# Optimization experiments

Hardware: AMD Instinct MI355X
Metric: run time of the kernel (lower is better)

The kernel has to match this reference:

```python
import jax, jax.numpy as jnp
from jax import lax
import numpy as np

CH = [1, 64, 64, 128, 128, 256, 256, 256, 512, 512, 512, 512, 512, 512]
POOL_AFTER = {2, 4, 7, 10, 13}  # VGG16: pool after layers 2,4,7,10,13
FLAT = 512 * 16 * 16  # 131072 after 5 pools of 512x512
MLP_DIMS = [(FLAT, 1024), (1024, 512), (512, 256), (256, 2)]


def _conv(x, w, b):
    # x: [B,C,H,W], w: [O,I,3,3] (OIHW), SAME padding, stride 1
    y = lax.conv_general_dilated(x, w, (1, 1), 'SAME',
                                 dimension_numbers=('NCHW', 'OIHW', 'NCHW'))
    return y + b[None, :, None, None]


def _pool(x):
    return lax.reduce_window(x, -jnp.inf, lax.max, (1, 1, 2, 2), (1, 1, 2, 2), 'VALID')


def setup_inputs() -> dict:
    key = jax.random.key(0)
    ks = jax.random.split(key, 40)
    inp = {}
    xr = jax.random.normal(ks[0], (2, 1, 512, 512), jnp.float32)
    keep = (jax.random.uniform(ks[1], (2, 1, 512, 512)) < 0.05).astype(jnp.float32)
    inp['x'] = xr * keep
    for i in range(13):
        cin, cout = CH[i], CH[i + 1]
        inp[f'w{i+1}'] = jax.random.normal(ks[2 + i], (cout, cin, 3, 3), jnp.float32) / np.sqrt(cin * 9.0)
        inp[f'b{i+1}'] = jnp.zeros((cout,), jnp.float32)
    for j, (a, b) in enumerate(MLP_DIMS):
        inp[f'fw{j+1}'] = jax.random.normal(ks[20 + j], (b, a), jnp.float32) / np.sqrt(float(a))
        inp[f'fb{j+1}'] = jnp.zeros((b,), jnp.float32)
    return inp


def reference(x, w1, b1, w2, b2, w3, b3, w4, b4, w5, b5, w6, b6, w7, b7,
              w8, b8, w9, b9, w10, b10, w11, b11, w12, b12, w13, b13,
              fw1, fb1, fw2, fb2, fw3, fb3, fw4, fb4):
    ws = [w1, w2, w3, w4, w5, w6, w7, w8, w9, w10, w11, w12, w13]
    bs = [b1, b2, b3, b4, b5, b6, b7, b8, b9, b10, b11, b12, b13]
    # active-site mask from nonzero input (spconv SparseConvTensor.from_dense)
    m = jnp.any(x != 0, axis=1, keepdims=True).astype(x.dtype)  # [B,1,H,W]
    h = x
    for i in range(13):
        # SubMConv2d: conv output (incl. bias) exists only at active sites -> mask
        h = jax.nn.relu(_conv(h, ws[i], bs[i]) * m)
        if (i + 1) in POOL_AFTER:
            # sparse maxpool == dense maxpool here (features >=0, inactive == 0)
            h = _pool(h)
            m = _pool(m)
    h = h.reshape(h.shape[0], -1)  # [B, 131072]
    h = jax.nn.relu(h @ fw1.T + fb1)
    h = jax.nn.relu(h @ fw2.T + fb2)
    h = jax.nn.relu(h @ fw3.T + fb3)
    return h @ fw4.T + fb4  # [B, 2]
```

## Files before the change

### kernel.cpp

```cpp
#include <hip/hip_runtime.h>
#include <hip/hip_bf16.h>
#include <cstddef>
#include <cstdint>

#define NB 2

#define NMAX512 32768
#define NMAX256 28672
#define NMAX128 20480
#define NMAX64  8192
#define NMAX32  2048

typedef __attribute__((ext_vector_type(8))) short bf8v;
typedef __attribute__((ext_vector_type(4))) float f32x4;
typedef __attribute__((ext_vector_type(16))) float f32x16;

static __device__ __forceinline__ unsigned short f2bf(float x) {
  __hip_bfloat16 h = __float2bfloat16(x);
  return *reinterpret_cast<unsigned short*>(&h);
}
static __device__ __forceinline__ float bf2f(unsigned short u) {
  __hip_bfloat16 h;
  *reinterpret_cast<unsigned short*>(&h) = u;
  return __bfloat162float(h);
}

__global__ __launch_bounds__(256) void build_l0_k(const float* __restrict__ x,
    int* __restrict__ list, int* __restrict__ im, float* __restrict__ f0,
    int* __restrict__ nact, int total, int nmax) {
  int i = blockIdx.x * 256 + threadIdx.x;
  bool act = false;
  float v = 0.f;
  if (i < total) { v = x[i]; act = (v != 0.f); }
  unsigned long long mb = __ballot(act);
  int lane = threadIdx.x & 63;
  int prefix = __popcll(mb & ((1ull << lane) - 1));
  int base = 0;
  if (lane == 0) base = atomicAdd(nact, __popcll(mb));
  base = __shfl(base, 0);
  if (i < total) {
    int idx = act ? (base + prefix) : -1;
    if (idx >= nmax) idx = -1;
    im[i] = idx;
    if (idx >= 0) {
      int b = i >> 18;
      int rem = i & 262143;
      list[idx] = (b << 20) | ((rem >> 9) << 10) | (rem & 511);
      f0[idx] = v;
    }
  }
}

__global__ __launch_bounds__(256) void build_pl_k(const int* __restrict__ imF,
    int* __restrict__ list, int* __restrict__ im, int* __restrict__ nact,
    int Hc, int nmax) {
  int total = NB * Hc * Hc;
  int i = blockIdx.x * 256 + threadIdx.x;
  bool act = false;
  int b = 0, y = 0, x = 0;
  int Hf = Hc * 2;
  if (i < total) {
    x = i % Hc; y = (i / Hc) % Hc; b = i / (Hc * Hc);
    const int* p = imF + ((size_t)b * Hf + 2 * y) * Hf + 2 * x;
    act = (p[0] >= 0) || (p[1] >= 0) || (p[Hf] >= 0) || (p[Hf + 1] >= 0);
  }
  unsigned long long mb = __ballot(act);
  int lane = threadIdx.x & 63;
  int prefix = __popcll(mb & ((1ull << lane) - 1));
  int base = 0;
  if (lane == 0) base = atomicAdd(nact, __popcll(mb));
  base = __shfl(base, 0);
  if (i < total) {
    int idx = act ? (base + prefix) : -1;
    if (idx >= nmax) idx = -1;
    im[i] = idx;
    if (idx >= 0) list[idx] = (b << 20) | (y << 10) | x;
  }
}

__global__ __launch_bounds__(256) void build_nbr_k(const int* __restrict__ list,
    const int* __restrict__ im, const int* __restrict__ nactp,
    int* __restrict__ nbr, int H, int nmax) {
  int i = blockIdx.x * 256 + threadIdx.x;
  if (i >= nactp[0]) return;
  int code = list[i];
  int b = code >> 20, y = (code >> 10) & 1023, x = code & 1023;
#pragma unroll
  for (int k = 0; k < 9; ++k) {
    int yy = y + k / 3 - 1, xx = x + k % 3 - 1;
    int v = -1;
    if (yy >= 0 && yy < H && xx >= 0 && xx < H)
      v = im[((size_t)b * H + yy) * H + xx];
    nbr[k * nmax + i] = v;
  }
}

__global__ __launch_bounds__(256) void transpose_k(const float* __restrict__ in,
                                                   float* __restrict__ out,
                                                   int R, int C) {
  __shared__ float tile[32][33];
  int bx = blockIdx.x * 32;
  int by = blockIdx.y * 32;
  int tx = threadIdx.x % 32, ty0 = threadIdx.x / 32;
  for (int ty = ty0; ty < 32; ty += 8) {
    int r = by + ty, c = bx + tx;
    tile[ty][tx] = (r < R && c < C) ? in[(size_t)r * C + c] : 0.f;
  }
  __syncthreads();
  for (int ty = ty0; ty < 32; ty += 8) {
    int r = bx + ty, c = by + tx;
    if (r < C && c < R) out[(size_t)r * R + c] = tile[tx][ty];
  }
}

__global__ __launch_bounds__(256) void wprep_k(const float* __restrict__ w,
                                               unsigned short* __restrict__ wx,
                                               int Cout, int Cin) {
  int i = blockIdx.x * 256 + threadIdx.x;
  if (i >= Cout * Cin) return;
  int oc = i / Cin, ci = i - oc * Cin;
  const float* src = w + ((size_t)oc * Cin + ci) * 9;
  const size_t sk = (size_t)Cout * Cin;
#pragma unroll
  for (int k = 0; k < 9; ++k) {
    float x = src[k];
    unsigned short h = f2bf(x);
    float r1 = x - bf2f(h);
    unsigned short m = f2bf(r1);
    float r2 = r1 - bf2f(m);
    wx[(size_t)k * sk + i] = h;
    wx[(size_t)(9 + k) * sk + i] = m;
    wx[(size_t)(18 + k) * sk + i] = f2bf(r2);
  }
}

template <int CC, int SITES, int OCB, int SPT, int OPT>
__global__ __launch_bounds__(256, 2) void gconv_k(
    const float* __restrict__ in, float* __restrict__ out,
    const float* __restrict__ wT, const float* __restrict__ bias,
    const int* __restrict__ nbr, const int* __restrict__ nactp,
    int Cin, int Cout, int Nmax, int cinCnt, int nocb) {
  constexpr int KSL = CC * 9;
  __shared__ int s_nbr[9][SITES];
  __shared__ float s_a[KSL][SITES];
  __shared__ float s_w[KSL][OCB];
  const int n = nactp[0];
  const int gid = blockIdx.x;
  const int xcd = gid & 7;
  const int pos = gid >> 3;
  const int ocbI = pos % nocb;
  const int sb = (pos / nocb) * 8 + xcd;
  const int base = sb * SITES;
  if (base >= n) return;
  const int ocb = ocbI * OCB;
  const int t = threadIdx.x;
  for (int s = t; s < 9 * SITES; s += 256) {
    int i = s % SITES, k = s / SITES;
    int gi = base + i;
    s_nbr[k][i] = (gi < n) ? nbr[k * Nmax + gi] : -1;
  }
  constexpr int OCG = OCB / OPT;
  const int oc0 = (t % OCG) * 4;
  const int si0 = (t / OCG) * SPT;
  float acc[SPT][OPT];
#pragma unroll
  for (int a = 0; a < SPT; ++a)
#pragma unroll
    for (int j = 0; j < OPT; ++j) acc[a][j] = 0.f;
  __syncthreads();
  const int nch = cinCnt / CC;
  for (int ch = 0; ch < nch; ++ch) {
    const int c0 = ch * CC;
    const float* wrow = wT + ((size_t)c0 * 9) * Cout + ocb;
    for (int s = t; s < KSL * (OCB / 4); s += 256) {
      int j4 = s % (OCB / 4), r = s / (OCB / 4);
      *(float4*)&s_w[r][j4 * 4] = *(const float4*)(wrow + (size_t)r * Cout + j4 * 4);
    }
    if constexpr (CC == 1) {
      for (int s = t; s < 9 * SITES; s += 256) {
        int i = s % SITES, k = s / SITES;
        int row = s_nbr[k][i];
        s_a[k][i] = (row >= 0) ? in[row] : 0.f;
      }
    } else {
      constexpr int H4 = CC / 4;
      for (int s = t; s < H4 * 9 * SITES; s += 256) {
        int i = s % SITES, m = s / SITES;
        int c4 = m % H4, k = m / H4;
        int row = s_nbr[k][i];
        float4 v = make_float4(0.f, 0.f, 0.f, 0.f);
        if (row >= 0)
          v = *(const float4*)(in + (size_t)row * Cin + c0 + c4 * 4);
        s_a[(c4 * 4 + 0) * 9 + k][i] = v.x;
        s_a[(c4 * 4 + 1) * 9 + k][i] = v.y;
        s_a[(c4 * 4 + 2) * 9 + k][i] = v.z;
        s_a[(c4 * 4 + 3) * 9 + k][i] = v.w;
      }
    }
    __syncthreads();
#pragma unroll
    for (int kk = 0; kk < KSL; ++kk) {
      float av[SPT];
      if constexpr (SPT == 4) {
        float4 a4 = *(const float4*)&s_a[kk][si0];
        av[0] = a4.x; av[1] = a4.y; av[2] = a4.z; av[3] = a4.w;
      } else {
        float2 a2 = *(const float2*)&s_a[kk][si0];
        av[0] = a2.x; av[1] = a2.y;
      }
      float wv[OPT];
      if constexpr (OPT == 8) {
        float4 w4a = *(const float4*)&s_w[kk][oc0];
        float4 w4b = *(const float4*)&s_w[kk][OCB / 2 + oc0];
        wv[0] = w4a.x; wv[1] = w4a.y; wv[2] = w4a.z; wv[3] = w4a.w;
        wv[4] = w4b.x; wv[5] = w4b.y; wv[6] = w4b.z; wv[7] = w4b.w;
      } else {
        float4 w4 = *(const float4*)&s_w[kk][oc0];
        wv[0] = w4.x; wv[1] = w4.y; wv[2] = w4.z; wv[3] = w4.w;
      }
#pragma unroll
      for (int a = 0; a < SPT; ++a)
#pragma unroll
        for (int j = 0; j < OPT; ++j)
          acc[a][j] = fmaf(av[a], wv[j], acc[a][j]);
    }
    __syncthreads();
  }
  float bz[OPT];
#pragma unroll
  for (int j = 0; j < OPT; ++j) {
    int oj = (OPT == 8) ? ((j < 4) ? (oc0 + j) : (OCB / 2 + oc0 + j - 4))
                        : (oc0 + j);
    bz[j] = bias[ocb + oj];
  }
#pragma unroll
  for (int a = 0; a < SPT; ++a) {
    int gi = base + si0 + a;
    if (gi < n) {
      float* po = out + (size_t)gi * Cout + ocb;
      if constexpr (OPT == 8) {
        float4 v0, v1;
        v0.x = fmaxf(acc[a][0] + bz[0], 0.f); v0.y = fmaxf(acc[a][1] + bz[1], 0.f);
        v0.z = fmaxf(acc[a][2] + bz[2], 0.f); v0.w = fmaxf(acc[a][3] + bz[3], 0.f);
        v1.x = fmaxf(acc[a][4] + bz[4], 0.f); v1.y = fmaxf(acc[a][5] + bz[5], 0.f);
        v1.z = fmaxf(acc[a][6] + bz[6], 0.f); v1.w = fmaxf(acc[a][7] + bz[7], 0.f);
        *(float4*)(po + oc0) = v0;
        *(float4*)(po + OCB / 2 + oc0) = v1;
      } else {
        float4 v;
        v.x = fmaxf(acc[a][0] + bz[0], 0.f); v.y = fmaxf(acc[a][1] + bz[1], 0.f);
        v.z = fmaxf(acc[a][2] + bz[2], 0.f); v.w = fmaxf(acc[a][3] + bz[3], 0.f);
        *(float4*)(po + oc0) = v;
      }
    }
  }
}

__global__ __launch_bounds__(256, 2) void gmfma32_k(
    const unsigned short* __restrict__ AH, const unsigned short* __restrict__ AM,
    const unsigned short* __restrict__ AL, float* __restrict__ outP,
    const unsigned short* __restrict__ WX, const int* __restrict__ nbr,
    const int* __restrict__ nactp, int Cin, int Cout, int Nmax, int cinCnt,
    int nocb) {
  __shared__ int s_nbr[9][128];
  __shared__ __align__(16) unsigned short s_a[3][2][128][8];
  __shared__ __align__(16) unsigned short s_w[3][2][128][8];
  const int n = nactp[0];
  const int gid = blockIdx.x;
  const int xcd = gid & 7, pos = gid >> 3;
  const int ocbI = pos % nocb;
  const int sb = (pos / nocb) * 8 + xcd;
  const int base = sb * 128;
  if (base >= n) return;
  const int ocb = ocbI * 128;
  const int t = threadIdx.x;
  for (int s = t; s < 1152; s += 256) {
    int i = s & 127, k = s >> 7;
    s_nbr[k][i] = (base + i < n) ? nbr[k * Nmax + base + i] : -1;
  }
  const int l = t & 63;
  const int wm = (t >> 6) & 1, wn = t >> 7;
  const int kh = l >> 5, lr = l & 31;
  const int skh = t >> 7, ssi = t & 127;
  f32x16 acc[2][2];
#pragma unroll
  for (int a = 0; a < 2; ++a)
#pragma unroll
    for (int b = 0; b < 2; ++b)
#pragma unroll
      for (int r = 0; r < 16; ++r) acc[a][b][r] = 0.f;
  __syncthreads();
  const int cinStart = blockIdx.z * cinCnt;
  const int nck = cinCnt >> 4;
  const size_t pstride = (size_t)9 * Cout * Cin;
  for (int k = 0; k < 9; ++k) {
    const unsigned short* Wk =
        WX + ((size_t)k * Cout + ocb + ssi) * Cin + skh * 8;
    for (int cc = 0; cc < nck; ++cc) {
      const int c0 = cinStart + (cc << 4);
      {
        const unsigned short* W0 = Wk + c0;
        *(float4*)&s_w[0][skh][ssi][0] = *(const float4*)(W0);
        *(float4*)&s_w[1][skh][ssi][0] = *(const float4*)(W0 + pstride);
        *(float4*)&s_w[2][skh][ssi][0] = *(const float4*)(W0 + 2 * pstride);
      }
      {
        int row = s_nbr[k][ssi];
        if (row >= 0) {
          const size_t off = (size_t)row * Cin + c0 + skh * 8;
          *(float4*)&s_a[0][skh][ssi][0] = *(const float4*)(AH + off);
          *(float4*)&s_a[1][skh][ssi][0] = *(const float4*)(AM + off);
          *(float4*)&s_a[2][skh][ssi][0] = *(const float4*)(AL + off);
        } else {
          float4 z = make_float4(0.f, 0.f, 0.f, 0.f);
          *(float4*)&s_a[0][skh][ssi][0] = z;
          *(float4*)&s_a[1][skh][ssi][0] = z;
          *(float4*)&s_a[2][skh][ssi][0] = z;
        }
      }
      __syncthreads();
      bf8v af[2][3], wf[2][3];
#pragma unroll
      for (int mi = 0; mi < 2; ++mi)
#pragma unroll
        for (int p = 0; p < 3; ++p)
          af[mi][p] = *(const bf8v*)&s_a[p][kh][wm * 64 + mi * 32 + lr][0];
#pragma unroll
      for (int ni = 0; ni < 2; ++ni)
#pragma unroll
        for (int p = 0; p < 3; ++p)
          wf[ni][p] = *(const bf8v*)&s_w[p][kh][wn * 64 + ni * 32 + lr][0];
#pragma unroll
      for (int mi = 0; mi < 2; ++mi)
#pragma unroll
        for (int ni = 0; ni < 2; ++ni) {
          f32x16 c = acc[mi][ni];
          c = __builtin_amdgcn_mfma_f32_32x32x16_bf16(af[mi][0], wf[ni][0], c, 0, 0, 0);
          c = __builtin_amdgcn_mfma_f32_32x32x16_bf16(af[mi][0], wf[ni][1], c, 0, 0, 0);
          c = __builtin_amdgcn_mfma_f32_32x32x16_bf16(af[mi][1], wf[ni][0], c, 0, 0, 0);
          c = __builtin_amdgcn_mfma_f32_32x32x16_bf16(af[mi][1], wf[ni][1], c, 0, 0, 0);
          c = __builtin_amdgcn_mfma_f32_32x32x16_bf16(af[mi][0], wf[ni][2], c, 0, 0, 0);
          c = __builtin_amdgcn_mfma_f32_32x32x16_bf16(af[mi][2], wf[ni][0], c, 0, 0, 0);
          acc[mi][ni] = c;
        }
      __syncthreads();
    }
  }
  float* ob = outP + (size_t)blockIdx.z * Nmax * Cout;
#pragma unroll
  for (int mi = 0; mi < 2; ++mi) {
    const int sbase = base + wm * 64 + mi * 32 + 4 * kh;
#pragma unroll
    for (int ni = 0; ni < 2; ++ni) {
      const int oc = ocb + wn * 64 + ni * 32 + lr;
#pragma unroll
      for (int reg = 0; reg < 16; ++reg) {
        int gi = sbase + (reg & 3) + 8 * (reg >> 2);
        if (gi < n) ob[(size_t)gi * Cout + oc] = acc[mi][ni][reg];
      }
    }
  }
}

__global__ __launch_bounds__(256) void combine_k(const float* __restrict__ P,
    float* __restrict__ out, const float* __restrict__ bias,
    const int* __restrict__ nactp, int C, int S, int sliceStride,
    unsigned short* __restrict__ oh, unsigned short* __restrict__ om,
    unsigned short* __restrict__ ol) {
  int tg = blockIdx.x * 256 + threadIdx.x;
  int cg = C >> 2;
  int j = tg / cg, c4 = tg % cg;
  if (j >= nactp[0]) return;
  size_t o = (size_t)j * C + c4 * 4;
  float4 v = *(const float4*)(bias + c4 * 4);
  for (int s = 0; s < S; ++s) {
    float4 u = *(const float4*)(P + (size_t)s * sliceStride + o);
    v.x += u.x; v.y += u.y; v.z += u.z; v.w += u.w;
  }
  v.x = fmaxf(v.x, 0.f); v.y = fmaxf(v.y, 0.f);
  v.z = fmaxf(v.z, 0.f); v.w = fmaxf(v.w, 0.f);
  if (out) *(float4*)(out + o) = v;
  if (oh) {
    const float* pv = &v.x;
#pragma unroll
    for (int u = 0; u < 4; ++u) {
      float y = pv[u];
      unsigned short h = f2bf(y);
      float r1 = y - bf2f(h);
      unsigned short m2 = f2bf(r1);
      float r2 = r1 - bf2f(m2);
      oh[o + u] = h; om[o + u] = m2; ol[o + u] = f2bf(r2);
    }
  }
}

__global__ __launch_bounds__(256) void pool_c_k(const float* __restrict__ inF,
    float* __restrict__ outF, const int* __restrict__ listC,
    const int* __restrict__ imF, const int* __restrict__ nactp, int Hf, int C,
    unsigned short* __restrict__ oh, unsigned short* __restrict__ om,
    unsigned short* __restrict__ ol) {
  int tg = blockIdx.x * 256 + threadIdx.x;
  int cg = C >> 2;
  int j = tg / cg, c4 = tg % cg;
  if (j >= nactp[0]) return;
  int code = listC[j];
  int b = code >> 20, Y = (code >> 10) & 1023, X = code & 1023;
  float4 v = make_float4(0.f, 0.f, 0.f, 0.f);
#pragma unroll
  for (int dy = 0; dy < 2; ++dy)
#pragma unroll
    for (int dx = 0; dx < 2; ++dx) {
      int ci = imF[((size_t)b * Hf + 2 * Y + dy) * Hf + 2 * X + dx];
      if (ci >= 0) {
        float4 u = *(const float4*)(inF + (size_t)ci * C + c4 * 4);
        v.x = fmaxf(v.x, u.x); v.y = fmaxf(v.y, u.y);
        v.z = fmaxf(v.z, u.z); v.w = fmaxf(v.w, u.w);
      }
    }
  size_t o = (size_t)j * C + c4 * 4;
  *(float4*)(outF + o) = v;
  if (oh) {
    const float* pv = &v.x;
#pragma unroll
    for (int u = 0; u < 4; ++u) {
      float y = pv[u];
      unsigned short h = f2bf(y);
      float r1 = y - bf2f(h);
      unsigned short m2 = f2bf(r1);
      float r2 = r1 - bf2f(m2);
      oh[o + u] = h; om[o + u] = m2; ol[o + u] = f2bf(r2);
    }
  }
}

__global__ __launch_bounds__(256) void pool_d_k(const float* __restrict__ inF,
    float* __restrict__ outD, const int* __restrict__ im32) {
  int tg = blockIdx.x * 256 + threadIdx.x;
  int c4 = tg & 127;
  int rest = tg >> 7;
  int X = rest & 15, Y = (rest >> 4) & 15, b = rest >> 8;
  float4 v = make_float4(0.f, 0.f, 0.f, 0.f);
#pragma unroll
  for (int dy = 0; dy < 2; ++dy)
#pragma unroll
    for (int dx = 0; dx < 2; ++dx) {
      int ci = im32[((size_t)b * 32 + 2 * Y + dy) * 32 + 2 * X + dx];
      if (ci >= 0) {
        float4 u = *(const float4*)(inF + (size_t)ci * 512 + c4 * 4);
        v.x = fmaxf(v.x, u.x); v.y = fmaxf(v.y, u.y);
        v.z = fmaxf(v.z, u.z); v.w = fmaxf(v.w, u.w);
      }
    }
  const float* pv = &v.x;
#pragma unroll
  for (int u = 0; u < 4; ++u) {
    int c = c4 * 4 + u;
    outD[(((size_t)b * 512 + c) * 16 + Y) * 16 + X] = pv[u];
  }
}

template <bool RELU>
__global__ __launch_bounds__(256) void fc_k(const float* __restrict__ in,
                                            const float* __restrict__ w,
                                            const float* __restrict__ bias,
                                            float* __restrict__ out, int K,
                                            int R) {
  const int r = blockIdx.x;
  const int t = threadIdx.x;
  const float* wr = w + (size_t)r * K;
  float a0 = 0.f, a1 = 0.f;
  for (int k = t * 4; k < K; k += 1024) {
    float4 wv = *(const float4*)(wr + k);
    float4 x0 = *(const float4*)(in + k);
    float4 x1 = *(const float4*)(in + K + k);
    a0 += wv.x * x0.x + wv.y * x0.y + wv.z * x0.z + wv.w * x0.w;
    a1 += wv.x * x1.x + wv.y * x1.y + wv.z * x1.z + wv.w * x1.w;
  }
#pragma unroll
  for (int off = 32; off > 0; off >>= 1) {
    a0 += __shfl_down(a0, off);
    a1 += __shfl_down(a1, off);
  }
  __shared__ float s0[4], s1[4];
  const int lane = t & 63, wid = t >> 6;
  if (lane == 0) { s0[wid] = a0; s1[wid] = a1; }
  __syncthreads();
  if (t == 0) {
    float v0 = s0[0] + s0[1] + s0[2] + s0[3] + bias[r];
    float v1 = s1[0] + s1[1] + s1[2] + s1[3] + bias[r];
    if (RELU) { v0 = fmaxf(v0, 0.f); v1 = fmaxf(v1, 0.f); }
    out[r] = v0;
    out[R + r] = v1;
  }
}

extern "C" void kernel_launch(void* const* d_in, const int* in_sizes, int n_in,
                              void* d_out, int out_size, void* d_ws,
                              size_t ws_size, hipStream_t stream) {
  (void)in_sizes; (void)n_in; (void)out_size; (void)ws_size;
  const float* x = (const float*)d_in[0];
  const float* Wc[14];
  const float* Bc[14];
  for (int i = 1; i <= 13; ++i) {
    Wc[i] = (const float*)d_in[2 * i - 1];
    Bc[i] = (const float*)d_in[2 * i];
  }
  const float* fw1 = (const float*)d_in[27];
  const float* fb1 = (const float*)d_in[28];
  const float* fw2 = (const float*)d_in[29];
  const float* fb2 = (const float*)d_in[30];
  const float* fw3 = (const float*)d_in[31];
  const float* fb3 = (const float*)d_in[32];
  const float* fw4 = (const float*)d_in[33];
  const float* fb4 = (const float*)d_in[34];

  static const int CH[14] = {1, 64, 64, 128, 128, 256, 256, 256,
                             512, 512, 512, 512, 512, 512};

  char* ws = (char*)d_ws;
  size_t cur = 0;
  auto alloc = [&](size_t bytes) {
    size_t o = cur;
    cur += (bytes + 255) & ~(size_t)255;
    return o;
  };
  size_t wtOff[5];
  for (int i = 1; i <= 4; ++i)
    wtOff[i] = alloc((size_t)CH[i] * CH[i - 1] * 9 * 4);
  float* wT[5];
  for (int i = 1; i <= 4; ++i) wT[i] = (float*)(ws + wtOff[i]);
  unsigned short* wX[14];
  for (int i = 5; i <= 13; ++i)
    wX[i] = (unsigned short*)(ws + alloc((size_t)3 * 9 * CH[i] * CH[i - 1] * 2));
  float* F0  = (float*)(ws + alloc((size_t)NMAX512 * 1 * 4));
  size_t a1Off = alloc((size_t)NMAX512 * 64 * 4);
  float* A1  = (float*)(ws + a1Off);
  float* Praw = A1;
  float* A2  = (float*)(ws + alloc((size_t)NMAX512 * 64 * 4));
  float* P2  = (float*)(ws + alloc((size_t)NMAX256 * 64 * 4));
  float* A3  = (float*)(ws + alloc((size_t)NMAX256 * 128 * 4));
  float* A4  = (float*)(ws + alloc((size_t)NMAX256 * 128 * 4));
  float* P4  = (float*)(ws + alloc((size_t)NMAX128 * 128 * 4));
  float* A5  = (float*)(ws + alloc((size_t)NMAX128 * 256 * 4));
  float* P7  = (float*)(ws + alloc((size_t)NMAX64 * 256 * 4));
  float* A8  = (float*)(ws + alloc((size_t)NMAX64 * 512 * 4));
  float* P10 = (float*)(ws + alloc((size_t)NMAX32 * 512 * 4));
  float* A11 = (float*)(ws + alloc((size_t)NMAX32 * 512 * 4));
  float* D13 = (float*)(ws + alloc((size_t)NB * 512 * 16 * 16 * 4));
  float* F1  = (float*)(ws + alloc(NB * 1024 * 4));
  float* F2  = (float*)(ws + alloc(NB * 512 * 4));
  float* F3  = (float*)(ws + alloc(NB * 256 * 4));
  const size_t PLE = (size_t)NMAX128 * 256;
  unsigned short* XH = (unsigned short*)(ws + alloc(PLE * 2));
  unsigned short* XM = (unsigned short*)(ws + alloc(PLE * 2));
  unsigned short* XL = (unsigned short*)(ws + alloc(PLE * 2));
  unsigned short* YH = (unsigned short*)(ws + alloc(PLE * 2));
  unsigned short* YM = (unsigned short*)(ws + alloc(PLE * 2));
  unsigned short* YL = (unsigned short*)(ws + alloc(PLE * 2));
  int* im512 = (int*)(ws + alloc((size_t)NB * 512 * 512 * 4));
  int* im256 = (int*)(ws + alloc((size_t)NB * 256 * 256 * 4));
  int* im128 = (int*)(ws + alloc((size_t)NB * 128 * 128 * 4));
  int* im64  = (int*)(ws + alloc((size_t)NB * 64 * 64 * 4));
  int* im32  = (int*)(ws + alloc((size_t)NB * 32 * 32 * 4));
  int* l512 = (int*)(ws + alloc((size_t)NMAX512 * 4));
  int* l256 = (int*)(ws + alloc((size_t)NMAX256 * 4));
  int* l128 = (int*)(ws + alloc((size_t)NMAX128 * 4));
  int* l64  = (int*)(ws + alloc((size_t)NMAX64 * 4));
  int* l32  = (int*)(ws + alloc((size_t)NMAX32 * 4));
  int* nb512 = (int*)(ws + alloc((size_t)9 * NMAX512 * 4));
  int* nb256 = (int*)(ws + alloc((size_t)9 * NMAX256 * 4));
  int* nb128 = (int*)(ws + alloc((size_t)9 * NMAX128 * 4));
  int* nb64  = (int*)(ws + alloc((size_t)9 * NMAX64 * 4));
  int* nb32  = (int*)(ws + alloc((size_t)9 * NMAX32 * 4));
  int* nact = (int*)(ws + alloc(256));

  const dim3 blk(256);
  hipMemsetAsync(nact, 0, 32, stream);

  hipLaunchKernelGGL(build_l0_k, dim3(2048), blk, 0, stream, x, l512, im512, F0, nact + 0, NB * 512 * 512, NMAX512);
  hipLaunchKernelGGL(build_pl_k, dim3(512), blk, 0, stream, im512, l256, im256, nact + 1, 256, NMAX256);
  hipLaunchKernelGGL(build_pl_k, dim3(128), blk, 0, stream, im256, l128, im128, nact + 2, 128, NMAX128);
  hipLaunchKernelGGL(build_pl_k, dim3(32), blk, 0, stream, im128, l64, im64, nact + 3, 64, NMAX64);
  hipLaunchKernelGGL(build_pl_k, dim3(8), blk, 0, stream, im64, l32, im32, nact + 4, 32, NMAX32);
  hipLaunchKernelGGL(build_nbr_k, dim3(NMAX512 / 256), blk, 0, stream, l512, im512, nact + 0, nb512, 512, NMAX512);
  hipLaunchKernelGGL(build_nbr_k, dim3(NMAX256 / 256), blk, 0, stream, l256, im256, nact + 1, nb256, 256, NMAX256);
  hipLaunchKernelGGL(build_nbr_k, dim3(NMAX128 / 256), blk, 0, stream, l128, im128, nact + 2, nb128, 128, NMAX128);
  hipLaunchKernelGGL(build_nbr_k, dim3(NMAX64 / 256), blk, 0, stream, l64, im64, nact + 3, nb64, 64, NMAX64);
  hipLaunchKernelGGL(build_nbr_k, dim3(NMAX32 / 256), blk, 0, stream, l32, im32, nact + 4, nb32, 32, NMAX32);

  for (int i = 1; i <= 4; ++i) {
    int R = CH[i], C = CH[i - 1] * 9;
    hipLaunchKernelGGL(transpose_k, dim3((C + 31) / 32, (R + 31) / 32), blk, 0,
                       stream, Wc[i], wT[i], R, C);
  }
  for (int i = 5; i <= 13; ++i) {
    int e = CH[i] * CH[i - 1];
    hipLaunchKernelGGL(wprep_k, dim3((e + 255) / 256), blk, 0, stream, Wc[i],
                       wX[i], CH[i], CH[i - 1]);
  }

  hipLaunchKernelGGL((gconv_k<1, 64, 64, 4, 4>), dim3(512, 1, 1), blk, 0, stream,
                     F0, A1, wT[1], Bc[1], nb512, nact + 0, 1, 64, NMAX512, 1, 1);
  hipLaunchKernelGGL((gconv_k<8, 64, 64, 4, 4>), dim3(512, 1, 1), blk, 0, stream,
                     A1, A2, wT[2], Bc[2], nb512, nact + 0, 64, 64, NMAX512, 64, 1);
  hipLaunchKernelGGL(pool_c_k, dim3(NMAX256 * 16 / 256), blk, 0, stream, A2, P2,
                     l256, im512, nact + 1, 512, 64, (unsigned short*)nullptr,
                     (unsigned short*)nullptr, (unsigned short*)nullptr);
  hipLaunchKernelGGL((gconv_k<8, 64, 128, 4, 8>), dim3(448, 1, 1), blk, 0, stream,
                     P2, A3, wT[3], Bc[3], nb256, nact + 1, 64, 128, NMAX256, 64, 1);
  hipLaunchKernelGGL((gconv_k<8, 64, 128, 4, 8>), dim3(448, 1, 1), blk, 0, stream,
                     A3, A4, wT[4], Bc[4], nb256, nact + 1, 128, 128, NMAX256, 128, 1);
  hipLaunchKernelGGL(pool_c_k, dim3(NMAX128 * 32 / 256), blk, 0, stream, A4, P4,
                     l128, im256, nact + 2, 256, 128, XH, XM, XL);

  unsigned short* NUL = nullptr;
  const int SL128 = NMAX128 * 256;
  const int SL64  = NMAX64 * 512;
  const int SL32  = NMAX32 * 512;
  hipLaunchKernelGGL(gmfma32_k, dim3(320, 1, 2), blk, 0, stream,
                     XH, XM, XL, Praw, wX[5], nb128, nact + 2, 128, 256, NMAX128, 64, 2);
  hipLaunchKernelGGL(combine_k, dim3(NMAX128 * 64 / 256), blk, 0, stream, Praw,
                     (float*)nullptr, Bc[5], nact + 2, 256, 2, SL128, YH, YM, YL);
  hipLaunchKernelGGL(gmfma32_k, dim3(320, 1, 2), blk, 0, stream,
                     YH, YM, YL, Praw, wX[6], nb128, nact + 2, 256, 256, NMAX128, 128, 2);
  hipLaunchKernelGGL(combine_k, dim3(NMAX128 * 64 / 256), blk, 0, stream, Praw,
                     (float*)nullptr, Bc[6], nact + 2, 256, 2, SL128, XH, XM, XL);
  hipLaunchKernelGGL(gmfma32_k, dim3(320, 1, 2), blk, 0, stream,
                     XH, XM, XL, Praw, wX[7], nb128, nact + 2, 256, 256, NMAX128, 128, 2);
  hipLaunchKernelGGL(combine_k, dim3(NMAX128 * 64 / 256), blk, 0, stream, Praw,
                     A5, Bc[7], nact + 2, 256, 2, SL128, NUL, NUL, NUL);
  hipLaunchKernelGGL(pool_c_k, dim3(NMAX64 * 64 / 256), blk, 0, stream, A5, P7,
                     l64, im128, nact + 3, 128, 256, XH, XM, XL);
  hipLaunchKernelGGL(gmfma32_k, dim3(256, 1, 2), blk, 0, stream,
                     XH, XM, XL, Praw, wX[8], nb64, nact + 3, 256, 512, NMAX64, 128, 4);
  hipLaunchKernelGGL(combine_k, dim3(NMAX64 * 128 / 256), blk, 0, stream, Praw,
                     (float*)nullptr, Bc[8], nact + 3, 512, 2, SL64, YH, YM, YL);
  hipLaunchKernelGGL(gmfma32_k, dim3(256, 1, 2), blk, 0, stream,
                     YH, YM, YL, Praw, wX[9], nb64, nact + 3, 512, 512, NMAX64, 256, 4);
  hipLaunchKernelGGL(combine_k, dim3(NMAX64 * 128 / 256), blk, 0, stream, Praw,
                     (float*)nullptr, Bc[9], nact + 3, 512, 2, SL64, XH, XM, XL);
  hipLaunchKernelGGL(gmfma32_k, dim3(256, 1, 2), blk, 0, stream,
                     XH, XM, XL, Praw, wX[10], nb64, nact + 3, 512, 512, NMAX64, 256, 4);
  hipLaunchKernelGGL(combine_k, dim3(NMAX64 * 128 / 256), blk, 0, stream, Praw,
                     A8, Bc[10], nact + 3, 512, 2, SL64, NUL, NUL, NUL);
  hipLaunchKernelGGL(pool_c_k, dim3(NMAX32 * 128 / 256), blk, 0, stream, A8, P10,
                     l32, im64, nact + 4, 64, 512, XH, XM, XL);
  hipLaunchKernelGGL(gmfma32_k, dim3(64, 1, 8), blk, 0, stream,
                     XH, XM, XL, Praw, wX[11], nb32, nact + 4, 512, 512, NMAX32, 64, 4);
  hipLaunchKernelGGL(combine_k, dim3(NMAX32 * 128 / 256), blk, 0, stream, Praw,
                     (float*)nullptr, Bc[11], nact + 4, 512, 8, SL32, YH, YM, YL);
  hipLaunchKernelGGL(gmfma32_k, dim3(64, 1, 8), blk, 0, stream,
                     YH, YM, YL, Praw, wX[12], nb32, nact + 4, 512, 512, NMAX32, 64, 4);
  hipLaunchKernelGGL(combine_k, dim3(NMAX32 * 128 / 256), blk, 0, stream, Praw,
                     (float*)nullptr, Bc[12], nact + 4, 512, 8, SL32, XH, XM, XL);
  hipLaunchKernelGGL(gmfma32_k, dim3(64, 1, 8), blk, 0, stream,
                     XH, XM, XL, Praw, wX[13], nb32, nact + 4, 512, 512, NMAX32, 64, 4);
  hipLaunchKernelGGL(combine_k, dim3(NMAX32 * 128 / 256), blk, 0, stream, Praw,
                     A11, Bc[13], nact + 4, 512, 8, SL32, NUL, NUL, NUL);
  hipLaunchKernelGGL(pool_d_k, dim3(256), blk, 0, stream, A11, D13, im32);

  hipLaunchKernelGGL((fc_k<true>), dim3(1024), blk, 0, stream, D13, fw1, fb1, F1, 131072, 1024);
  hipLaunchKernelGGL((fc_k<true>), dim3(512), blk, 0, stream, F1, fw2, fb2, F2, 1024, 512);
  hipLaunchKernelGGL((fc_k<true>), dim3(256), blk, 0, stream, F2, fw3, fb3, F3, 512, 256);
  hipLaunchKernelGGL((fc_k<false>), dim3(2), blk, 0, stream, F3, fw4, fb4, (float*)d_out, 256, 2);
}
```

Baseline: 2.272 ms.

## Prefetch next K-chunk into registers in gather-MFMA conv and raise split-K for 64-res layers

Measured after the change: 2.179 ms (median of 3 runs). -4.1%, faster.

```diff
diff --git a/kernel.cpp b/kernel.cpp
--- a/kernel.cpp
+++ b/kernel.cpp
@@ -292,59 +292,76 @@
   __syncthreads();
   const int cinStart = blockIdx.z * cinCnt;
   const int nck = cinCnt >> 4;
+  const int np = 9 * nck;
   const size_t pstride = (size_t)9 * Cout * Cin;
-  for (int k = 0; k < 9; ++k) {
-    const unsigned short* Wk =
-        WX + ((size_t)k * Cout + ocb + ssi) * Cin + skh * 8;
-    for (int cc = 0; cc < nck; ++cc) {
-      const int c0 = cinStart + (cc << 4);
-      {
-        const unsigned short* W0 = Wk + c0;
-        *(float4*)&s_w[0][skh][ssi][0] = *(const float4*)(W0);
-        *(float4*)&s_w[1][skh][ssi][0] = *(const float4*)(W0 + pstride);
-        *(float4*)&s_w[2][skh][ssi][0] = *(const float4*)(W0 + 2 * pstride);
-      }
-      {
-        int row = s_nbr[k][ssi];
-        if (row >= 0) {
-          const size_t off = (size_t)row * Cin + c0 + skh * 8;
-          *(float4*)&s_a[0][skh][ssi][0] = *(const float4*)(AH + off);
-          *(float4*)&s_a[1][skh][ssi][0] = *(const float4*)(AM + off);
-          *(float4*)&s_a[2][skh][ssi][0] = *(const float4*)(AL + off);
-        } else {
-          float4 z = make_float4(0.f, 0.f, 0.f, 0.f);
-          *(float4*)&s_a[0][skh][ssi][0] = z;
-          *(float4*)&s_a[1][skh][ssi][0] = z;
-          *(float4*)&s_a[2][skh][ssi][0] = z;
-        }
-      }
-      __syncthreads();
-      bf8v af[2][3], wf[2][3];
-#pragma unroll
-      for (int mi = 0; mi < 2; ++mi)
-#pragma unroll
-        for (int p = 0; p < 3; ++p)
-          af[mi][p] = *(const bf8v*)&s_a[p][kh][wm * 64 + mi * 32 + lr][0];
-#pragma unroll
-      for (int ni = 0; ni < 2; ++ni)
-#pragma unroll
-        for (int p = 0; p < 3; ++p)
-          wf[ni][p] = *(const bf8v*)&s_w[p][kh][wn * 64 + ni * 32 + lr][0];
-#pragma unroll
-      for (int mi = 0; mi < 2; ++mi)
-#pragma unroll
-        for (int ni = 0; ni < 2; ++ni) {
-          f32x16 c = acc[mi][ni];
-          c = __builtin_amdgcn_mfma_f32_32x32x16_bf16(af[mi][0], wf[ni][0], c, 0, 0, 0);
-          c = __builtin_amdgcn_mfma_f32_32x32x16_bf16(af[mi][0], wf[ni][1], c, 0, 0, 0);
-          c = __builtin_amdgcn_mfma_f32_32x32x16_bf16(af[mi][1], wf[ni][0], c, 0, 0, 0);
-          c = __builtin_amdgcn_mfma_f32_32x32x16_bf16(af[mi][1], wf[ni][1], c, 0, 0, 0);
-          c = __builtin_amdgcn_mfma_f32_32x32x16_bf16(af[mi][0], wf[ni][2], c, 0, 0, 0);
-          c = __builtin_amdgcn_mfma_f32_32x32x16_bf16(af[mi][2], wf[ni][0], c, 0, 0, 0);
-          acc[mi][ni] = c;
-        }
-      __syncthreads();
-    }
+  const size_t kstrideW = (size_t)Cout * Cin;
+  const unsigned short* Wth = WX + ((size_t)(ocb + ssi)) * Cin + skh * 8;
+  const float4 z4 = make_float4(0.f, 0.f, 0.f, 0.f);
+  float4 pw0, pw1, pw2, pa0, pa1, pa2;
+  {
+    const unsigned short* W0 = Wth + cinStart;
+    pw0 = *(const float4*)(W0);
+    pw1 = *(const float4*)(W0 + pstride);
+    pw2 = *(const float4*)(W0 + 2 * pstride);
+    int row = s_nbr[0][ssi];
+    if (row >= 0) {
+      const size_t off = (size_t)row * Cin + cinStart + skh * 8;
+      pa0 = *(const float4*)(AH + off);
+      pa1 = *(const float4*)(AM + off);
+      pa2 = *(const float4*)(AL + off);
+    } else { pa0 = z4; pa1 = z4; pa2 = z4; }
+  }
+  int k = 0, cc = 0;
+  for (int ph = 0; ph < np; ++ph) {
+    __syncthreads();
+    *(float4*)&s_w[0][skh][ssi][0] = pw0;
+    *(float4*)&s_w[1][skh][ssi][0] = pw1;
+    *(float4*)&s_w[2][skh][ssi][0] = pw2;
+    *(float4*)&s_a[0][skh][ssi][0] = pa0;
+    *(float4*)&s_a[1][skh][ssi][0] = pa1;
+    *(float4*)&s_a[2][skh][ssi][0] = pa2;
+    __syncthreads();
+    int cc2 = cc + 1, k2 = k;
+    if (cc2 == nck) { cc2 = 0; ++k2; }
+    if (ph + 1 < np) {
+      const int c0n = cinStart + (cc2 << 4);
+      const unsigned short* W0 = Wth + (size_t)k2 * kstrideW + c0n;
+      pw0 = *(const float4*)(W0);
+      pw1 = *(const float4*)(W0 + pstride);
+      pw2 = *(const float4*)(W0 + 2 * pstride);
+      int row = s_nbr[k2][ssi];
+      if (row >= 0) {
+        const size_t off = (size_t)row * Cin + c0n + skh * 8;
+        pa0 = *(const float4*)(AH + off);
+        pa1 = *(const float4*)(AM + off);
+        pa2 = *(const float4*)(AL + off);
+      } else { pa0 = z4; pa1 = z4; pa2 = z4; }
+    }
+    k = k2; cc = cc2;
+    bf8v af[2][3], wf[2][3];
+#pragma unroll
+    for (int mi = 0; mi < 2; ++mi)
+#pragma unroll
+      for (int p = 0; p < 3; ++p)
+        af[mi][p] = *(const bf8v*)&s_a[p][kh][wm * 64 + mi * 32 + lr][0];
+#pragma unroll
+    for (int ni = 0; ni < 2; ++ni)
+#pragma unroll
+      for (int p = 0; p < 3; ++p)
+        wf[ni][p] = *(const bf8v*)&s_w[p][kh][wn * 64 + ni * 32 + lr][0];
+#pragma unroll
+    for (int mi = 0; mi < 2; ++mi)
+#pragma unroll
+      for (int ni = 0; ni < 2; ++ni) {
+        f32x16 c = acc[mi][ni];
+        c = __builtin_amdgcn_mfma_f32_32x32x16_bf16(af[mi][0], wf[ni][0], c, 0, 0, 0);
+        c = __builtin_amdgcn_mfma_f32_32x32x16_bf16(af[mi][0], wf[ni][1], c, 0, 0, 0);
+        c = __builtin_amdgcn_mfma_f32_32x32x16_bf16(af[mi][1], wf[ni][0], c, 0, 0, 0);
+        c = __builtin_amdgcn_mfma_f32_32x32x16_bf16(af[mi][1], wf[ni][1], c, 0, 0, 0);
+        c = __builtin_amdgcn_mfma_f32_32x32x16_bf16(af[mi][0], wf[ni][2], c, 0, 0, 0);
+        c = __builtin_amdgcn_mfma_f32_32x32x16_bf16(af[mi][2], wf[ni][0], c, 0, 0, 0);
+        acc[mi][ni] = c;
+      }
   }
   float* ob = outP + (size_t)blockIdx.z * Nmax * Cout;
 #pragma unroll
@@ -631,18 +648,18 @@
                      A5, Bc[7], nact + 2, 256, 2, SL128, NUL, NUL, NUL);
   hipLaunchKernelGGL(pool_c_k, dim3(NMAX64 * 64 / 256), blk, 0, stream, A5, P7,
                      l64, im128, nact + 3, 128, 256, XH, XM, XL);
-  hipLaunchKernelGGL(gmfma32_k, dim3(256, 1, 2), blk, 0, stream,
-                     XH, XM, XL, Praw, wX[8], nb64, nact + 3, 256, 512, NMAX64, 128, 4);
+  hipLaunchKernelGGL(gmfma32_k, dim3(256, 1, 4), blk, 0, stream,
+                     XH, XM, XL, Praw, wX[8], nb64, nact + 3, 256, 512, NMAX64, 64, 4);
   hipLaunchKernelGGL(combine_k, dim3(NMAX64 * 128 / 256), blk, 0, stream, Praw,
-                     (float*)nullptr, Bc[8], nact + 3, 512, 2, SL64, YH, YM, YL);
-  hipLaunchKernelGGL(gmfma32_k, dim3(256, 1, 2), blk, 0, stream,
-                     YH, YM, YL, Praw, wX[9], nb64, nact + 3, 512, 512, NMAX64, 256, 4);
+                     (float*)nullptr, Bc[8], nact + 3, 512, 4, SL64, YH, YM, YL);
+  hipLaunchKernelGGL(gmfma32_k, dim3(256, 1, 4), blk, 0, stream,
+                     YH, YM, YL, Praw, wX[9], nb64, nact + 3, 512, 512, NMAX64, 128, 4);
   hipLaunchKernelGGL(combine_k, dim3(NMAX64 * 128 / 256), blk, 0, stream, Praw,
-                     (float*)nullptr, Bc[9], nact + 3, 512, 2, SL64, XH, XM, XL);
-  hipLaunchKernelGGL(gmfma32_k, dim3(256, 1, 2), blk, 0, stream,
-                     XH, XM, XL, Praw, wX[10], nb64, nact + 3, 512, 512, NMAX64, 256, 4);
+                     (float*)nullptr, Bc[9], nact + 3, 512, 4, SL64, XH, XM, XL);
+  hipLaunchKernelGGL(gmfma32_k, dim3(256, 1, 4), blk, 0, stream,
+                     XH, XM, XL, Praw, wX[10], nb64, nact + 3, 512, 512, NMAX64, 128, 4);
   hipLaunchKernelGGL(combine_k, dim3(NMAX64 * 128 / 256), blk, 0, stream, Praw,
-                     A8, Bc[10], nact + 3, 512, 2, SL64, NUL, NUL, NUL);
+                     A8, Bc[10], nact + 3, 512, 4, SL64, NUL, NUL, NUL);
   hipLaunchKernelGGL(pool_c_k, dim3(NMAX32 * 128 / 256), blk, 0, stream, A8, P10,
                      l32, im64, nact + 4, 64, 512, XH, XM, XL);
   hipLaunchKernelGGL(gmfma32_k, dim3(64, 1, 8), blk, 0, stream,
```

## Double-buffer gmfma32 loads via direct global-to-LDS and widen split-K for 64-res layers

Applied to the files above, without the earlier changes.

Result: faster. 2.181 ms (-4.0%).

```diff
diff --git a/kernel.cpp b/kernel.cpp
--- a/kernel.cpp
+++ b/kernel.cpp
@@ -14,6 +14,11 @@
 typedef __attribute__((ext_vector_type(8))) short bf8v;
 typedef __attribute__((ext_vector_type(4))) float f32x4;
 typedef __attribute__((ext_vector_type(16))) float f32x16;
+
+#define GLL16(g, l)                                                         \
+  __builtin_amdgcn_global_load_lds(                                         \
+      (const __attribute__((address_space(1))) void*)(g),                   \
+      (__attribute__((address_space(3))) void*)(l), 16, 0, 0)
 
 static __device__ __forceinline__ unsigned short f2bf(float x) {
   __hip_bfloat16 h = __float2bfloat16(x);
@@ -260,11 +265,11 @@
     const unsigned short* __restrict__ AH, const unsigned short* __restrict__ AM,
     const unsigned short* __restrict__ AL, float* __restrict__ outP,
     const unsigned short* __restrict__ WX, const int* __restrict__ nbr,
-    const int* __restrict__ nactp, int Cin, int Cout, int Nmax, int cinCnt,
-    int nocb) {
+    const int* __restrict__ nactp, const unsigned short* __restrict__ zb,
+    int Cin, int Cout, int Nmax, int cinCnt, int nocb) {
   __shared__ int s_nbr[9][128];
-  __shared__ __align__(16) unsigned short s_a[3][2][128][8];
-  __shared__ __align__(16) unsigned short s_w[3][2][128][8];
+  __shared__ __align__(16) unsigned short s_a[2][3][2][128][8];
+  __shared__ __align__(16) unsigned short s_w[2][3][2][128][8];
   const int n = nactp[0];
   const int gid = blockIdx.x;
   const int xcd = gid & 7, pos = gid >> 3;
@@ -282,6 +287,7 @@
   const int wm = (t >> 6) & 1, wn = t >> 7;
   const int kh = l >> 5, lr = l & 31;
   const int skh = t >> 7, ssi = t & 127;
+  const int wrb = ((t >> 6) & 1) << 6;
   f32x16 acc[2][2];
 #pragma unroll
   for (int a = 0; a < 2; ++a)
@@ -292,60 +298,71 @@
   __syncthreads();
   const int cinStart = blockIdx.z * cinCnt;
   const int nck = cinCnt >> 4;
+  const int np = 9 * nck;
   const size_t pstride = (size_t)9 * Cout * Cin;
-  for (int k = 0; k < 9; ++k) {
-    const unsigned short* Wk =
-        WX + ((size_t)k * Cout + ocb + ssi) * Cin + skh * 8;
-    for (int cc = 0; cc < nck; ++cc) {
-      const int c0 = cinStart + (cc << 4);
-      {
-        const unsigned short* W0 = Wk + c0;
-        *(float4*)&s_w[0][skh][ssi][0] = *(const float4*)(W0);
-        *(float4*)&s_w[1][skh][ssi][0] = *(const float4*)(W0 + pstride);
-        *(float4*)&s_w[2][skh][ssi][0] = *(const float4*)(W0 + 2 * pstride);
-      }
-      {
-        int row = s_nbr[k][ssi];
-        if (row >= 0) {
-          const size_t off = (size_t)row * Cin + c0 + skh * 8;
-          *(float4*)&s_a[0][skh][ssi][0] = *(const float4*)(AH + off);
-          *(float4*)&s_a[1][skh][ssi][0] = *(const float4*)(AM + off);
-          *(float4*)&s_a[2][skh][ssi][0] = *(const float4*)(AL + off);
-        } else {
-          float4 z = make_float4(0.f, 0.f, 0.f, 0.f);
-          *(float4*)&s_a[0][skh][ssi][0] = z;
-          *(float4*)&s_a[1][skh][ssi][0] = z;
-          *(float4*)&s_a[2][skh][ssi][0] = z;
-        }
-      }
-      __syncthreads();
-      bf8v af[2][3], wf[2][3];
-#pragma unroll
-      for (int mi = 0; mi < 2; ++mi)
-#pragma unroll
-        for (int p = 0; p < 3; ++p)
-          af[mi][p] = *(const bf8v*)&s_a[p][kh][wm * 64 + mi * 32 + lr][0];
-#pragma unroll
-      for (int ni = 0; ni < 2; ++ni)
-#pragma unroll
-        for (int p = 0; p < 3; ++p)
-          wf[ni][p] = *(const bf8v*)&s_w[p][kh][wn * 64 + ni * 32 + lr][0];
-#pragma unroll
-      for (int mi = 0; mi < 2; ++mi)
-#pragma unroll
-        for (int ni = 0; ni < 2; ++ni) {
-          f32x16 c = acc[mi][ni];
-          c = __builtin_amdgcn_mfma_f32_32x32x16_bf16(af[mi][0], wf[ni][0], c, 0, 0, 0);
-          c = __builtin_amdgcn_mfma_f32_32x32x16_bf16(af[mi][0], wf[ni][1], c, 0, 0, 0);
-          c = __builtin_amdgcn_mfma_f32_32x32x16_bf16(af[mi][1], wf[ni][0], c, 0, 0, 0);
-          c = __builtin_amdgcn_mfma_f32_32x32x16_bf16(af[mi][1], wf[ni][1], c, 0, 0, 0);
-          c = __builtin_amdgcn_mfma_f32_32x32x16_bf16(af[mi][0], wf[ni][2], c, 0, 0, 0);
-          c = __builtin_amdgcn_mfma_f32_32x32x16_bf16(af[mi][2], wf[ni][0], c, 0, 0, 0);
-          acc[mi][ni] = c;
-        }
-      __syncthreads();
-    }
-  }
+  const size_t kstrideW = (size_t)Cout * Cin;
+  const unsigned short* Wth = WX + (size_t)(ocb + ssi) * Cin + skh * 8;
+  int ik = 0, icc = 0;
+#define ISSUE_CHUNK(slotv)                                                  \
+  {                                                                         \
+    const int c0i = cinStart + (icc << 4);                                  \
+    const unsigned short* W0 = Wth + (size_t)ik * kstrideW + c0i;           \
+    GLL16(W0,               &s_w[slotv][0][skh][wrb][0]);                   \
+    GLL16(W0 + pstride,     &s_w[slotv][1][skh][wrb][0]);                   \
+    GLL16(W0 + 2 * pstride, &s_w[slotv][2][skh][wrb][0]);                   \
+    int rowi = s_nbr[ik][ssi];                                              \
+    size_t offi = 0;                                                        \
+    if (rowi >= 0) offi = (size_t)rowi * Cin + c0i + skh * 8;               \
+    const unsigned short* a0 = (rowi >= 0) ? (AH + offi) : zb;              \
+    const unsigned short* a1 = (rowi >= 0) ? (AM + offi) : zb;              \
+    const unsigned short* a2 = (rowi >= 0) ? (AL + offi) : zb;              \
+    GLL16(a0, &s_a[slotv][0][skh][wrb][0]);                                 \
+    GLL16(a1, &s_a[slotv][1][skh][wrb][0]);                                 \
+    GLL16(a2, &s_a[slotv][2][skh][wrb][0]);                                 \
+    if (++icc == nck) { icc = 0; ++ik; }                                    \
+  }
+  ISSUE_CHUNK(0);
+  ISSUE_CHUNK(1);
+  for (int ph = 0; ph < np; ++ph) {
+    const int slot = ph & 1;
+    if (ph + 2 < np) {
+      asm volatile("s_waitcnt vmcnt(6)" ::: "memory");
+    } else {
+      asm volatile("s_waitcnt vmcnt(0)" ::: "memory");
+    }
+    __builtin_amdgcn_s_barrier();
+    asm volatile("" ::: "memory");
+    bf8v af[2][3], wf[2][3];
+#pragma unroll
+    for (int mi = 0; mi < 2; ++mi)
+#pragma unroll
+      for (int p = 0; p < 3; ++p)
+        af[mi][p] = *(const bf8v*)&s_a[slot][p][kh][wm * 64 + mi * 32 + lr][0];
+#pragma unroll
+    for (int ni = 0; ni < 2; ++ni)
+#pragma unroll
+      for (int p = 0; p < 3; ++p)
+        wf[ni][p] = *(const bf8v*)&s_w[slot][p][kh][wn * 64 + ni * 32 + lr][0];
+#pragma unroll
+    for (int mi = 0; mi < 2; ++mi)
+#pragma unroll
+      for (int ni = 0; ni < 2; ++ni) {
+        f32x16 c = acc[mi][ni];
+        c = __builtin_amdgcn_mfma_f32_32x32x16_bf16(af[mi][0], wf[ni][0], c, 0, 0, 0);
+        c = __builtin_amdgcn_mfma_f32_32x32x16_bf16(af[mi][0], wf[ni][1], c, 0, 0, 0);
+        c = __builtin_amdgcn_mfma_f32_32x32x16_bf16(af[mi][1], wf[ni][0], c, 0, 0, 0);
+        c = __builtin_amdgcn_mfma_f32_32x32x16_bf16(af[mi][1], wf[ni][1], c, 0, 0, 0);
+        c = __builtin_amdgcn_mfma_f32_32x32x16_bf16(af[mi][0], wf[ni][2], c, 0, 0, 0);
+        c = __builtin_amdgcn_mfma_f32_32x32x16_bf16(af[mi][2], wf[ni][0], c, 0, 0, 0);
+        acc[mi][ni] = c;
+      }
+    asm volatile("" ::: "memory");
+    __builtin_amdgcn_s_barrier();
+    if (ph + 2 < np) {
+      ISSUE_CHUNK(slot);
+    }
+  }
+#undef ISSUE_CHUNK
   float* ob = outP + (size_t)blockIdx.z * Nmax * Cout;
 #pragma unroll
   for (int mi = 0; mi < 2; ++mi) {
@@ -573,9 +590,11 @@
   int* nb64  = (int*)(ws + alloc((size_t)9 * NMAX64 * 4));
   int* nb32  = (int*)(ws + alloc((size_t)9 * NMAX32 * 4));
   int* nact = (int*)(ws + alloc(256));
+  unsigned short* zbuf = (unsigned short*)(ws + alloc(256));
 
   const dim3 blk(256);
   hipMemsetAsync(nact, 0, 32, stream);
+  hipMemsetAsync(zbuf, 0, 256, stream);
 
   hipLaunchKernelGGL(build_l0_k, dim3(2048), blk, 0, stream, x, l512, im512, F0, nact + 0, NB * 512 * 512, NMAX512);
   hipLaunchKernelGGL(build_pl_k, dim3(512), blk, 0, stream, im512, l256, im256, nact + 1, 256, NMAX256);
@@ -618,43 +637,43 @@
   const int SL64  = NMAX64 * 512;
   const int SL32  = NMAX32 * 512;
   hipLaunchKernelGGL(gmfma32_k, dim3(320, 1, 2), blk, 0, stream,
-                     XH, XM, XL, Praw, wX[5], nb128, nact + 2, 128, 256, NMAX128, 64, 2);
+                     XH, XM, XL, Praw, wX[5], nb128, nact + 2, zbuf, 128, 256, NMAX128, 64, 2);
   hipLaunchKernelGGL(combine_k, dim3(NMAX128 * 64 / 256), blk, 0, stream, Praw,
                      (float*)nullptr, Bc[5], nact + 2, 256, 2, SL128, YH, YM, YL);
   hipLaunchKernelGGL(gmfma32_k, dim3(320, 1, 2), blk, 0, stream,
-                     YH, YM, YL, Praw, wX[6], nb128, nact + 2, 256, 256, NMAX128, 128, 2);
+                     YH, YM, YL, Praw, wX[6], nb128, nact + 2, zbuf, 256, 256, NMAX128, 128, 2);
   hipLaunchKernelGGL(combine_k, dim3(NMAX128 * 64 / 256), blk, 0, stream, Praw,
                      (float*)nullptr, Bc[6], nact + 2, 256, 2, SL128, XH, XM, XL);
   hipLaunchKernelGGL(gmfma32_k, dim3(320, 1, 2), blk, 0, stream,
-                     XH, XM, XL, Praw, wX[7], nb128, nact + 2, 256, 256, NMAX128, 128, 2);
+                     XH, XM, XL, Praw, wX[7], nb128, nact + 2, zbuf, 256, 256, NMAX128, 128, 2);
   hipLaunchKernelGGL(combine_k, dim3(NMAX128 * 64 / 256), blk, 0, stream, Praw,
                      A5, Bc[7], nact + 2, 256, 2, SL128, NUL, NUL, NUL);
   hipLaunchKernelGGL(pool_c_k, dim3(NMAX64 * 64 / 256), blk, 0, stream, A5, P7,
                      l64, im128, nact + 3, 128, 256, XH, XM, XL);
-  hipLaunchKernelGGL(gmfma32_k, dim3(256, 1, 2), blk, 0, stream,
-                     XH, XM, XL, Praw, wX[8], nb64, nact + 3, 256, 512, NMAX64, 128, 4);
+  hipLaunchKernelGGL(gmfma32_k, dim3(256, 1, 4), blk, 0, stream,
+                     XH, XM, XL, Praw, wX[8], nb64, nact + 3, zbuf, 256, 512, NMAX64, 64, 4);
   hipLaunchKernelGGL(combine_k, dim3(NMAX64 * 128 / 256), blk, 0, stream, Praw,
-                     (float*)nullptr, Bc[8], nact + 3, 512, 2, SL64, YH, YM, YL);
-  hipLaunchKernelGGL(gmfma32_k, dim3(256, 1, 2), blk, 0, stream,
-                     YH, YM, YL, Praw, wX[9], nb64, nact + 3, 512, 512, NMAX64, 256, 4);
+                     (float*)nullptr, Bc[8], nact + 3, 512, 4, SL64, YH, YM, YL);
+  hipLaunchKernelGGL(gmfma32_k, dim3(256, 1, 4), blk, 0, stream,
+                     YH, YM, YL, Praw, wX[9], nb64, nact + 3, zbuf, 512, 512, NMAX64, 128, 4);
   hipLaunchKernelGGL(combine_k, dim3(NMAX64 * 128 / 256), blk, 0, stream, Praw,
-                     (float*)nullptr, Bc[9], nact + 3, 512, 2, SL64, XH, XM, XL);
-  hipLaunchKernelGGL(gmfma32_k, dim3(256, 1, 2), blk, 0, stream,
-                     XH, XM, XL, Praw, wX[10], nb64, nact + 3, 512, 512, NMAX64, 256, 4);
+                     (float*)nullptr, Bc[9], nact + 3, 512, 4, SL64, XH, XM, XL);
+  hipLaunchKernelGGL(gmfma32_k, dim3(256, 1, 4), blk, 0, stream,
+                     XH, XM, XL, Praw, wX[10], nb64, nact + 3, zbuf, 512, 512, NMAX64, 128, 4);
   hipLaunchKernelGGL(combine_k, dim3(NMAX64 * 128 / 256), blk, 0, stream, Praw,
-                     A8, Bc[10], nact + 3, 512, 2, SL64, NUL, NUL, NUL);
+                     A8, Bc[10], nact + 3, 512, 4, SL64, NUL, NUL, NUL);
   hipLaunchKernelGGL(pool_c_k, dim3(NMAX32 * 128 / 256), blk, 0, stream, A8, P10,
                      l32, im64, nact + 4, 64, 512, XH, XM, XL);
   hipLaunchKernelGGL(gmfma32_k, dim3(64, 1, 8), blk, 0, stream,
-                     XH, XM, XL, Praw, wX[11], nb32, nact + 4, 512, 512, NMAX32, 64, 4);
+                     XH, XM, XL, Praw, wX[11], nb32, nact + 4, zbuf, 512, 512, NMAX32, 64, 4);
   hipLaunchKernelGGL(combine_k, dim3(NMAX32 * 128 / 256), blk, 0, stream, Praw,
                      (float*)nullptr, Bc[11], nact + 4, 512, 8, SL32, YH, YM, YL);
   hipLaunchKernelGGL(gmfma32_k, dim3(64, 1, 8), blk, 0, stream,
-                     YH, YM, YL, Praw, wX[12], nb32, nact + 4, 512, 512, NMAX32, 64, 4);
+                     YH, YM, YL, Praw, wX[12], nb32, nact + 4, zbuf, 512, 512, NMAX32, 64, 4);
   hipLaunchKernelGGL(combine_k, dim3(NMAX32 * 128 / 256), blk, 0, stream, Praw,
                      (float*)nullptr, Bc[12], nact + 4, 512, 8, SL32, XH, XM, XL);
   hipLaunchKernelGGL(gmfma32_k, dim3(64, 1, 8), blk, 0, stream,
-                     XH, XM, XL, Praw, wX[13], nb32, nact + 4, 512, 512, NMAX32, 64, 4);
+                     XH, XM, XL, Praw, wX[13], nb32, nact + 4, zbuf, 512, 512, NMAX32, 64, 4);
   hipLaunchKernelGGL(combine_k, dim3(NMAX32 * 128 / 256), blk, 0, stream, Praw,
                      A11, Bc[13], nact + 4, 512, 8, SL32, NUL, NUL, NUL);
   hipLaunchKernelGGL(pool_d_k, dim3(256), blk, 0, stream, A11, D13, im32);
```
